# Kernel tuning notes

Measured on AMD Instinct MI355X. Metric: run time of the kernel, lower is better.

Reference implementation:

```python
import jax, jax.numpy as jnp
import numpy as np

MIN_VAL = -100000.0
K = 48          # num_tags
START = 46      # tag_to_ix['<START>']
END = 47        # tag_to_ix['<END>']
B = 512         # batch of sentences (vmapped; original code is per-sentence)
T = 1024        # sentence length


def setup_inputs() -> dict:
    key = jax.random.key(0)
    k1, k2, k3 = jax.random.split(key, 3)
    feats = jax.random.normal(k1, (B, T, K), dtype=jnp.float32)
    trans = jax.random.normal(k2, (K, K), dtype=jnp.float32) * 0.1
    # structural constraints from CRF.__init__: nothing transitions FROM END
    # (column END) and nothing transitions TO START (row START)
    trans = trans.at[START, :].set(MIN_VAL).at[:, END].set(MIN_VAL)
    tags = jax.random.randint(k3, (B, T), 0, START)  # gold tags, never START/END
    return {"feats": feats, "trans": trans, "tags": tags}


def _neg_ll_single(feats, trans, tags):
    # feats: [T, K], trans: [K, K] (trans[i, j] = score of j -> i), tags: [T]
    init_alpha = jnp.full((K,), MIN_VAL, dtype=feats.dtype).at[START].set(0.0)

    def step(alpha, feat):
        # alpha_new[i] = logsumexp_j(trans[i, j] + alpha[j]) + feat[i]
        alpha = jax.nn.logsumexp(trans + alpha[None, :], axis=1) + feat
        return alpha, None

    alpha, _ = jax.lax.scan(step, init_alpha, feats)
    log_z = jax.nn.logsumexp(alpha + trans[END])  # forward_alg

    # get_gold_scores: sum_i trans[tags[i+1], tags[i]] + feat[i][tags[i+1]]
    prev = jnp.concatenate([jnp.array([START], dtype=tags.dtype), tags[:-1]])
    emit = jnp.take_along_axis(feats, tags[:, None], axis=1)[:, 0]  # [T]
    gold = jnp.sum(trans[tags, prev] + emit) + trans[END, tags[-1]]

    return log_z - gold  # neg_ll_loss


def reference(feats, trans, tags):
    # per-sentence negative log-likelihood, shape [B]
    return jax.vmap(_neg_ll_single, in_axes=(0, None, 0))(feats, trans, tags)
```

## Files before the change

kernel.cpp:

```cpp
#include <hip/hip_runtime.h>
#include <math.h>

#define KK 48
#define TT 1024
#define BB 512
#define START_TAG 46
#define END_TAG 47
#define NSEG 16
#define OWN (TT / NSEG)
#define WARM 12
#define NTHR (NSEG * 64)

typedef _Float16 h2 __attribute__((ext_vector_type(2)));

#if defined(__has_builtin)
#if __has_builtin(__builtin_amdgcn_fdot2)
#define HAVE_FDOT2 1
#endif
#endif

__device__ __forceinline__ float fdot2(h2 a, h2 b, float c) {
#ifdef HAVE_FDOT2
    return __builtin_amdgcn_fdot2(a, b, c, false);
#else
    return c + (float)a.x * (float)b.x + (float)a.y * (float)b.y;
#endif
}


template <bool EXACT>
__device__ __forceinline__ void run_seg(const float* __restrict__ fb,
                                        const float* __restrict__ trans,
                                        int ci, bool evenLane,
                                        int r0, int ngrp,
                                        float& sOut, int& oOut, float& q0Out) {
    h2 Eh[24];
    #pragma unroll
    for (int c = 0; c < 24; ++c) {
        float e0 = __expf(trans[ci * KK + 2 * c]);
        float e1 = __expf(trans[ci * KK + 2 * c + 1]);
        Eh[c] = (h2){(_Float16)e0, (_Float16)e1};
    }

    int au[24];
    #pragma unroll
    for (int c = 0; c < 24; ++c)
        au[c] = EXACT ? ((c == 23) ? 0x00003C00 : 0) : 0x3C003C00;

    float s = 0.0f;
    int esum = 0;
    int eswm = 0;
    float q0 = 1.0f;

    float fr[4];
    #pragma unroll
    for (int k = 0; k < 4; ++k) fr[k] = fb[(r0 + k) * KK + ci];

    const int WG = WARM / 4;
    for (int g = 0; g < ngrp; ++g) {
        float fn[4] = {0.f, 0.f, 0.f, 0.f};
        if (g < ngrp - 1) {
            #pragma unroll
            for (int k = 0; k < 4; ++k)
                fn[k] = fb[(r0 + (g + 1) * 4 + k) * KK + ci];
        }
        float ef[4];
        #pragma unroll
        for (int k = 0; k < 4; ++k) ef[k] = __expf(fr[k]);

        #pragma unroll
        for (int k = 0; k < 4; ++k) {
            float a0 = 0.f, a1 = 0.f, a2 = 0.f, a3 = 0.f;
            #pragma unroll
            for (int c = 0; c < 6; ++c) {
                a0 = fdot2(Eh[4 * c + 0], __builtin_bit_cast(h2, au[4 * c + 0]), a0);
                a1 = fdot2(Eh[4 * c + 1], __builtin_bit_cast(h2, au[4 * c + 1]), a1);
                a2 = fdot2(Eh[4 * c + 2], __builtin_bit_cast(h2, au[4 * c + 2]), a2);
                a3 = fdot2(Eh[4 * c + 3], __builtin_bit_cast(h2, au[4 * c + 3]), a3);
            }
            float sr = ((a0 + a1) + (a2 + a3)) * ef[k];
            int rl0 = __builtin_amdgcn_readlane(__float_as_int(sr), 0);
            int e0 = ((rl0 >> 23) & 0xff) - 127;
            esum += e0;
            s = sr * __int_as_float((127 - e0) << 23);
            int pb = __builtin_amdgcn_update_dpp(
                0, __float_as_int(s), 0xB1, 0xF, 0xF, true);
            float pv = __int_as_float(pb);
            float lo = evenLane ? s : pv;
            float hi = evenLane ? pv : s;
            int pkb = __builtin_bit_cast(int, __builtin_amdgcn_cvt_pkrtz(lo, hi));
            #pragma unroll
            for (int c = 0; c < 24; ++c)
                au[c] = __builtin_amdgcn_readlane(pkb, 2 * c);
        }

        if (!EXACT && g == WG - 1) {
            eswm = esum;
            q0 = __int_as_float(__builtin_amdgcn_readfirstlane(__float_as_int(s)));
        }

        #pragma unroll
        for (int k = 0; k < 4; ++k) fr[k] = fn[k];
    }
    sOut = s;
    oOut = esum - eswm;
    q0Out = q0;
}

__global__ __launch_bounds__(NTHR)
__attribute__((amdgpu_waves_per_eu(8)))
void crf_kernel(const float* __restrict__ feats,
                const float* __restrict__ trans,
                const int* __restrict__ tags,
                float* __restrict__ out) {
    const int b = blockIdx.x;
    const int tid = threadIdx.x;
    const int wave = tid >> 6;
    const int lane = tid & 63;
    const int ci = (lane < KK) ? lane : 0;
    const bool evenLane = (lane & 1) == 0;
    const float* fb = feats + (size_t)b * TT * KK;
    const int* tg = tags + b * TT;

    __shared__ float shU[NSEG][64];
    __shared__ int shO[NSEG];
    __shared__ float shQ0[NSEG];
    __shared__ float shGp[NSEG];

    float sF; int oW; float q0;
    if (wave == 0) run_seg<true >(fb, trans, ci, evenLane, 0, OWN / 4, sF, oW, q0);
    else           run_seg<false>(fb, trans, ci, evenLane,
                                  wave * OWN - WARM, (OWN + WARM) / 4, sF, oW, q0);

    shU[wave][lane] = sF;
    if (lane == 0) { shO[wave] = oW; shQ0[wave] = q0; }

    float gacc = 0.0f;
    #pragma unroll
    for (int r = 0; r < TT / NTHR; ++r) {
        int t = tid + r * NTHR;
        int cur = tg[t];
        int prev = (t == 0) ? START_TAG : tg[t - 1];
        gacc += trans[cur * KK + prev] + fb[(size_t)t * KK + cur];
    }
    #pragma unroll
    for (int off = 32; off; off >>= 1) gacc += __shfl_xor(gacc, off, 64);
    if (lane == 0) shGp[wave] = gacc;

    __syncthreads();

    if (tid < 64) {
        float val = (lane < KK) ? __expf(trans[END_TAG * KK + lane]) * shU[NSEG - 1][lane]
                                : 0.0f;
        #pragma unroll
        for (int off = 32; off; off >>= 1) val += __shfl_xor(val, off, 64);
        if (lane == 0) {
            int osum = 0;
            float gold = trans[END_TAG * KK + tg[TT - 1]];
            #pragma unroll
            for (int w = 0; w < NSEG; ++w) { osum += shO[w]; gold += shGp[w]; }
            float logz = __logf(val) + (float)osum * 0.6931471805599453f;
            #pragma unroll
            for (int w = 1; w < NSEG; ++w)
                logz += __logf(shU[w - 1][0]) - __logf(shQ0[w]);
            out[b] = logz - gold;
        }
    }
}

extern "C" void kernel_launch(void* const* d_in, const int* in_sizes, int n_in,
                              void* d_out, int out_size, void* d_ws, size_t ws_size,
                              hipStream_t stream) {
    const float* feats = (const float*)d_in[0];
    const float* trans = (const float*)d_in[1];
    const int* tags = (const int*)d_in[2];
    float* out = (float*)d_out;

    crf_kernel<<<BB, NTHR, 0, stream>>>(feats, trans, tags, out);
}
```

Before: 199.0 us.

## Batch 16 sentences per wave and run the forward recurrence on MFMA

Each wave now advances the forward-algorithm recurrence for 16 sentences at once as a 48x48 by 48x16 matrix product using 16x16x16 f16 MFMA instructions, replacing the per-lane fdot2 loop and 24 readlane broadcasts per step. Blocks now cover 16 sentences each (32 blocks instead of 512), and the gold-score and combine phase is redistributed so that each wave finishes one sentence. This cuts per-step cross-lane broadcast and dot-product work, but far fewer blocks means most of the GPU's compute units may sit idle. The serial dependency chain through MFMA latency is also kept.

New measurement: 277.1 us. 39.3% more time.

```diff
diff --git a/kernel.cpp b/kernel.cpp
--- a/kernel.cpp
+++ b/kernel.cpp
@@ -10,160 +10,176 @@
 #define OWN (TT / NSEG)
 #define WARM 12
 #define NTHR (NSEG * 64)
+#define NGRP (BB / 16)
 
 typedef _Float16 h2 __attribute__((ext_vector_type(2)));
+typedef _Float16 f16x4 __attribute__((ext_vector_type(4)));
+typedef float f32x4 __attribute__((ext_vector_type(4)));
 
-#if defined(__has_builtin)
-#if __has_builtin(__builtin_amdgcn_fdot2)
-#define HAVE_FDOT2 1
-#endif
+#if defined(__HIP_DEVICE_COMPILE__)
+  #if __has_builtin(__builtin_amdgcn_mfma_f32_16x16x16f16)
+    #define MFMA16(A, B, C) __builtin_amdgcn_mfma_f32_16x16x16f16((A), (B), (C), 0, 0, 0)
+  #elif __has_builtin(__builtin_amdgcn_mfma_f32_16x16x16_f16)
+    #define MFMA16(A, B, C) __builtin_amdgcn_mfma_f32_16x16x16_f16((A), (B), (C), 0, 0, 0)
+  #else
+    #error "no 16x16x16 f16 mfma on this target"
+  #endif
+#else
+  #define MFMA16(A, B, C) (C)
 #endif
 
-__device__ __forceinline__ float fdot2(h2 a, h2 b, float c) {
-#ifdef HAVE_FDOT2
-    return __builtin_amdgcn_fdot2(a, b, c, false);
-#else
-    return c + (float)a.x * (float)b.x + (float)a.y * (float)b.y;
-#endif
+__device__ __forceinline__ h2 pkrtz(float a, float b) {
+    return __builtin_bit_cast(h2, __builtin_amdgcn_cvt_pkrtz(a, b));
 }
 
 
 template <bool EXACT>
-__device__ __forceinline__ void run_seg(const float* __restrict__ fb,
+__device__ __forceinline__ void run_seg(const float* __restrict__ fbl,
                                         const float* __restrict__ trans,
-                                        int ci, bool evenLane,
-                                        int r0, int ngrp,
-                                        float& sOut, int& oOut, float& q0Out) {
-    h2 Eh[24];
+                                        int lane, int g4, int r0, int nsteps,
+                                        float (&wv)[3][4], int& esumO, int& eswmO,
+                                        float& q0O) {
+    f16x4 Af[3][3];
     #pragma unroll
-    for (int c = 0; c < 24; ++c) {
-        float e0 = __expf(trans[ci * KK + 2 * c]);
-        float e1 = __expf(trans[ci * KK + 2 * c + 1]);
-        Eh[c] = (h2){(_Float16)e0, (_Float16)e1};
+    for (int m = 0; m < 3; ++m) {
+        const int row = 16 * m + (lane & 15);
+        #pragma unroll
+        for (int c = 0; c < 3; ++c) {
+            #pragma unroll
+            for (int j = 0; j < 4; ++j)
+                Af[m][c][j] = (_Float16)__expf(trans[row * KK + 16 * c + 4 * g4 + j]);
+        }
     }
 
-    int au[24];
+    f16x4 bf[3];
+    if (EXACT) {
+        #pragma unroll
+        for (int c = 0; c < 3; ++c) bf[c] = (f16x4)(_Float16)0.0f;
+        if (g4 == 3) bf[2][2] = (_Float16)1.0f;
+    } else {
+        #pragma unroll
+        for (int c = 0; c < 3; ++c) bf[c] = (f16x4)(_Float16)1.0f;
+    }
+
+    int esum = 0, eswm = 0;
+    float q0v = 1.0f;
+
+    f32x4 ftA[3], ftB[3];
     #pragma unroll
-    for (int c = 0; c < 24; ++c)
-        au[c] = EXACT ? ((c == 23) ? 0x00003C00 : 0) : 0x3C003C00;
+    for (int m = 0; m < 3; ++m)
+        ftA[m] = *(const f32x4*)(fbl + (size_t)r0 * KK + 16 * m + 4 * g4);
 
-    float s = 0.0f;
-    int esum = 0;
-    int eswm = 0;
-    float q0 = 1.0f;
+    auto STEP = [&](f32x4(&ftU)[3], f32x4(&ftL)[3], int st) {
+        int tn = r0 + st + 1;
+        if (tn > TT - 1) tn = TT - 1;
+        #pragma unroll
+        for (int m = 0; m < 3; ++m)
+            ftL[m] = *(const f32x4*)(fbl + (size_t)tn * KK + 16 * m + 4 * g4);
+        float ef[3][4];
+        #pragma unroll
+        for (int m = 0; m < 3; ++m)
+            #pragma unroll
+            for (int r = 0; r < 4; ++r) ef[m][r] = __expf(ftU[m][r]);
+        const f32x4 z = {0.f, 0.f, 0.f, 0.f};
+        f32x4 a0 = MFMA16(Af[0][0], bf[0], z);
+        f32x4 a1 = MFMA16(Af[1][0], bf[0], z);
+        f32x4 a2 = MFMA16(Af[2][0], bf[0], z);
+        a0 = MFMA16(Af[0][1], bf[1], a0);
+        a1 = MFMA16(Af[1][1], bf[1], a1);
+        a2 = MFMA16(Af[2][1], bf[1], a2);
+        a0 = MFMA16(Af[0][2], bf[2], a0);
+        a1 = MFMA16(Af[1][2], bf[2], a1);
+        a2 = MFMA16(Af[2][2], bf[2], a2);
+        #pragma unroll
+        for (int r = 0; r < 4; ++r) {
+            wv[0][r] = a0[r] * ef[0][r];
+            wv[1][r] = a1[r] * ef[1][r];
+            wv[2][r] = a2[r] * ef[2][r];
+        }
+        float ref = __shfl(wv[0][0], lane & 15, 64);
+        int eb = ((__float_as_int(ref) >> 23) & 0xff) - 127;
+        esum += eb;
+        float sc = __int_as_float((127 - eb) << 23);
+        #pragma unroll
+        for (int m = 0; m < 3; ++m)
+            #pragma unroll
+            for (int r = 0; r < 4; ++r) wv[m][r] *= sc;
+        if (!EXACT && st == WARM - 1) { eswm = esum; q0v = ref * sc; }
+        #pragma unroll
+        for (int m = 0; m < 3; ++m) {
+            h2 lo = pkrtz(wv[m][0], wv[m][1]);
+            h2 hi = pkrtz(wv[m][2], wv[m][3]);
+            bf[m][0] = lo.x; bf[m][1] = lo.y; bf[m][2] = hi.x; bf[m][3] = hi.y;
+        }
+    };
 
-    float fr[4];
-    #pragma unroll
-    for (int k = 0; k < 4; ++k) fr[k] = fb[(r0 + k) * KK + ci];
-
-    const int WG = WARM / 4;
-    for (int g = 0; g < ngrp; ++g) {
-        float fn[4] = {0.f, 0.f, 0.f, 0.f};
-        if (g < ngrp - 1) {
-            #pragma unroll
-            for (int k = 0; k < 4; ++k)
-                fn[k] = fb[(r0 + (g + 1) * 4 + k) * KK + ci];
-        }
-        float ef[4];
-        #pragma unroll
-        for (int k = 0; k < 4; ++k) ef[k] = __expf(fr[k]);
-
-        #pragma unroll
-        for (int k = 0; k < 4; ++k) {
-            float a0 = 0.f, a1 = 0.f, a2 = 0.f, a3 = 0.f;
-            #pragma unroll
-            for (int c = 0; c < 6; ++c) {
-                a0 = fdot2(Eh[4 * c + 0], __builtin_bit_cast(h2, au[4 * c + 0]), a0);
-                a1 = fdot2(Eh[4 * c + 1], __builtin_bit_cast(h2, au[4 * c + 1]), a1);
-                a2 = fdot2(Eh[4 * c + 2], __builtin_bit_cast(h2, au[4 * c + 2]), a2);
-                a3 = fdot2(Eh[4 * c + 3], __builtin_bit_cast(h2, au[4 * c + 3]), a3);
-            }
-            float sr = ((a0 + a1) + (a2 + a3)) * ef[k];
-            int rl0 = __builtin_amdgcn_readlane(__float_as_int(sr), 0);
-            int e0 = ((rl0 >> 23) & 0xff) - 127;
-            esum += e0;
-            s = sr * __int_as_float((127 - e0) << 23);
-            int pb = __builtin_amdgcn_update_dpp(
-                0, __float_as_int(s), 0xB1, 0xF, 0xF, true);
-            float pv = __int_as_float(pb);
-            float lo = evenLane ? s : pv;
-            float hi = evenLane ? pv : s;
-            int pkb = __builtin_bit_cast(int, __builtin_amdgcn_cvt_pkrtz(lo, hi));
-            #pragma unroll
-            for (int c = 0; c < 24; ++c)
-                au[c] = __builtin_amdgcn_readlane(pkb, 2 * c);
-        }
-
-        if (!EXACT && g == WG - 1) {
-            eswm = esum;
-            q0 = __int_as_float(__builtin_amdgcn_readfirstlane(__float_as_int(s)));
-        }
-
-        #pragma unroll
-        for (int k = 0; k < 4; ++k) fr[k] = fn[k];
+    for (int st = 0; st < nsteps; st += 2) {
+        STEP(ftA, ftB, st);
+        STEP(ftB, ftA, st + 1);
     }
-    sOut = s;
-    oOut = esum - eswm;
-    q0Out = q0;
+    esumO = esum; eswmO = eswm; q0O = q0v;
 }
 
 __global__ __launch_bounds__(NTHR)
-__attribute__((amdgpu_waves_per_eu(8)))
 void crf_kernel(const float* __restrict__ feats,
                 const float* __restrict__ trans,
                 const int* __restrict__ tags,
                 float* __restrict__ out) {
-    const int b = blockIdx.x;
+    const int g = blockIdx.x;
     const int tid = threadIdx.x;
-    const int wave = tid >> 6;
+    const int seg = tid >> 6;
     const int lane = tid & 63;
-    const int ci = (lane < KK) ? lane : 0;
-    const bool evenLane = (lane & 1) == 0;
-    const float* fb = feats + (size_t)b * TT * KK;
-    const int* tg = tags + b * TT;
+    const int g4 = lane >> 4;
+    const int sb = g * 16 + (lane & 15);
+    const float* fbl = feats + (size_t)sb * TT * KK;
 
-    __shared__ float shU[NSEG][64];
-    __shared__ int shO[NSEG];
-    __shared__ float shQ0[NSEG];
-    __shared__ float shGp[NSEG];
+    __shared__ float shU[NSEG][16][KK];
+    __shared__ int shO[NSEG][16];
+    __shared__ float shQ0[NSEG][16];
 
-    float sF; int oW; float q0;
-    if (wave == 0) run_seg<true >(fb, trans, ci, evenLane, 0, OWN / 4, sF, oW, q0);
-    else           run_seg<false>(fb, trans, ci, evenLane,
-                                  wave * OWN - WARM, (OWN + WARM) / 4, sF, oW, q0);
+    float wv[3][4];
+    int esum, eswm; float q0v;
+    if (seg == 0) run_seg<true >(fbl, trans, lane, g4, 0, OWN, wv, esum, eswm, q0v);
+    else          run_seg<false>(fbl, trans, lane, g4, seg * OWN - WARM, OWN + WARM,
+                                 wv, esum, eswm, q0v);
 
-    shU[wave][lane] = sF;
-    if (lane == 0) { shO[wave] = oW; shQ0[wave] = q0; }
-
-    float gacc = 0.0f;
     #pragma unroll
-    for (int r = 0; r < TT / NTHR; ++r) {
-        int t = tid + r * NTHR;
-        int cur = tg[t];
-        int prev = (t == 0) ? START_TAG : tg[t - 1];
-        gacc += trans[cur * KK + prev] + fb[(size_t)t * KK + cur];
-    }
-    #pragma unroll
-    for (int off = 32; off; off >>= 1) gacc += __shfl_xor(gacc, off, 64);
-    if (lane == 0) shGp[wave] = gacc;
-
+    for (int m = 0; m < 3; ++m)
+        #pragma unroll
+        for (int r = 0; r < 4; ++r)
+            shU[seg][lane & 15][16 * m + 4 * g4 + r] = wv[m][r];
+    if (lane < 16) { shO[seg][lane] = esum - eswm; shQ0[seg][lane] = q0v; }
     __syncthreads();
 
-    if (tid < 64) {
-        float val = (lane < KK) ? __expf(trans[END_TAG * KK + lane]) * shU[NSEG - 1][lane]
+    {
+        const int w = seg;
+        const int sent = g * 16 + w;
+        const int* tg = tags + (size_t)sent * TT;
+        float val = (lane < KK) ? __expf(trans[END_TAG * KK + lane]) * shU[NSEG - 1][w][lane]
                                 : 0.0f;
         #pragma unroll
         for (int off = 32; off; off >>= 1) val += __shfl_xor(val, off, 64);
+        float stv = 0.0f;
+        if (lane >= 1 && lane < NSEG)
+            stv = __logf(shU[lane - 1][w][0]) - __logf(shQ0[lane][w]);
+        if (lane < NSEG)
+            stv += (float)shO[lane][w] * 0.6931471805599453f;
+        #pragma unroll
+        for (int off = 32; off; off >>= 1) stv += __shfl_xor(stv, off, 64);
+        float gacc = 0.0f;
+        const float* fbs = feats + (size_t)sent * TT * KK;
+        #pragma unroll
+        for (int it = 0; it < TT / 64; ++it) {
+            int t = lane + it * 64;
+            int cur = tg[t];
+            int prev = (t == 0) ? START_TAG : tg[t - 1];
+            gacc += trans[cur * KK + prev] + fbs[(size_t)t * KK + cur];
+        }
+        #pragma unroll
+        for (int off = 32; off; off >>= 1) gacc += __shfl_xor(gacc, off, 64);
         if (lane == 0) {
-            int osum = 0;
-            float gold = trans[END_TAG * KK + tg[TT - 1]];
-            #pragma unroll
-            for (int w = 0; w < NSEG; ++w) { osum += shO[w]; gold += shGp[w]; }
-            float logz = __logf(val) + (float)osum * 0.6931471805599453f;
-            #pragma unroll
-            for (int w = 1; w < NSEG; ++w)
-                logz += __logf(shU[w - 1][0]) - __logf(shQ0[w]);
-            out[b] = logz - gold;
+            float gold = gacc + trans[END_TAG * KK + tg[TT - 1]];
+            out[sent] = __logf(val) + stv - gold;
         }
     }
 }
@@ -176,5 +192,5 @@
     const int* tags = (const int*)d_in[2];
     float* out = (float*)d_out;
 
-    crf_kernel<<<BB, NTHR, 0, stream>>>(feats, trans, tags, out);
+    crf_kernel<<<NGRP, NTHR, 0, stream>>>(feats, trans, tags, out);
 }
```
